# Performance work log

Hardware: AMD Instinct MI355X
Metric: run time of the kernel (lower is better)

## Reference

```python
import jax, jax.numpy as jnp
import numpy as np

B, S, HID = 2, 2048, 2048
H, HKV, D = 16, 4, 128

def _rope(x, cos, sin):
    # x: [B,h,S,D]; cos/sin: [1,1,S,D//2]
    d = x.shape[-1] // 2
    x1, x2 = x[..., :d], x[..., d:]
    y1 = x1 * cos + x2 * sin
    y2 = -x1 * sin + x2 * cos
    return jnp.concatenate([y1, y2], axis=-1)

def _rmsnorm(x):
    eps = jnp.finfo(x.dtype).eps
    return x * jax.lax.rsqrt(jnp.mean(jnp.square(x), axis=-1, keepdims=True) + eps)

def setup_inputs() -> dict:
    key = jax.random.key(0)
    ks = jax.random.split(key, 5)
    x = jax.random.normal(ks[0], (B, S, HID), dtype=jnp.float32)
    # realistic rotary tables
    half = D // 2
    inv_freq = 1.0 / (10000.0 ** (jnp.arange(half, dtype=jnp.float32) / half))
    t = jnp.arange(S, dtype=jnp.float32)
    freqs = t[:, None] * inv_freq[None, :]            # [S, D//2]
    cos = jnp.cos(freqs)[None, None]                  # [1,1,S,D//2]
    sin = jnp.sin(freqs)[None, None]
    s = 0.02
    Wq = jax.random.normal(ks[1], (H * D, HID), dtype=jnp.float32) * s
    Wk = jax.random.normal(ks[2], (HKV * D, HID), dtype=jnp.float32) * s
    Wv = jax.random.normal(ks[3], (HKV * D, HID), dtype=jnp.float32) * s
    Wo = jax.random.normal(ks[4], (HID, H * D), dtype=jnp.float32) * s
    return {"x": x, "cos": cos, "sin": sin, "Wq": Wq, "Wk": Wk, "Wv": Wv, "Wo": Wo}

def reference(x, cos, sin, Wq, Wk, Wv, Wo):
    b, s, _ = x.shape
    rep = H // HKV
    q = (x @ Wq.T).reshape(b, s, H, D).transpose(0, 2, 1, 3)      # [B,H,S,D]
    k = (x @ Wk.T).reshape(b, s, HKV, D).transpose(0, 2, 1, 3)    # [B,Hkv,S,D]
    v = (x @ Wv.T).reshape(b, s, HKV, D).transpose(0, 2, 1, 3)
    k = jnp.repeat(k, rep, axis=1)                                # GQA expand
    v = jnp.repeat(v, rep, axis=1)
    q = _rmsnorm(_rope(q, cos, sin))
    k = _rmsnorm(_rope(k, cos, sin))
    scores = jnp.einsum('bhqd,bhkd->bhqk', q, k) * (D ** -0.5)
    causal = jnp.tril(jnp.ones((s, s), dtype=bool))
    scores = jnp.where(causal, scores, -jnp.inf)
    attn = jax.nn.softmax(scores, axis=-1)
    out = jnp.einsum('bhqk,bhkd->bhqd', attn, v)                  # [B,H,S,D]
    out = out.transpose(0, 2, 1, 3).reshape(b, s, H * D)
    return out @ Wo.T
```

## Files before the change

### kernel.cpp

```cpp
#include <hip/hip_runtime.h>
#include <hip/hip_bf16.h>

#define B_  2
#define S_  2048
#define HID_ 2048
#define H_  16
#define HKV_ 4
#define D_  128

typedef __bf16 bf16_t;
typedef bf16_t bf16x8 __attribute__((ext_vector_type(8)));
typedef float f32x4 __attribute__((ext_vector_type(4)));

typedef __attribute__((address_space(3))) unsigned int lds_u32_t;
typedef const __attribute__((address_space(1))) unsigned int glob_u32_t;

__device__ __forceinline__ void gl2lds16(const bf16_t* g, bf16_t* l) {
    __builtin_amdgcn_global_load_lds((glob_u32_t*)g, (lds_u32_t*)l, 16, 0, 0);
}

__device__ __forceinline__ unsigned packbf2(float a, float b) {
    union { bf16_t h[2]; unsigned u; } p;
    p.h[0] = (bf16_t)a;
    p.h[1] = (bf16_t)b;
    return p.u;
}

__global__ void detect_dtype(const unsigned* __restrict__ x, int* __restrict__ flag) {
    int lane = threadIdx.x;
    int c = 0;
#pragma unroll
    for (int i = 0; i < 16; ++i) {
        unsigned w = x[lane * 16 + i];
        unsigned e = (w >> 7) & 0xFF;
        c += (e >= 117 && e <= 137) ? 1 : 0;
    }
#pragma unroll
    for (int m = 1; m < 64; m <<= 1) c += __shfl_xor(c, m, 64);
    if (lane == 0) *flag = (c >= 512) ? 1 : 0;
}

struct Cseg { const void* src; bf16_t* dst; int n8; };

__global__ __launch_bounds__(256) void convert_bf16(Cseg s0, Cseg s1, Cseg s2, Cseg s3,
                                                    const int* __restrict__ flagp) {
    Cseg s = (blockIdx.y == 0) ? s0 : (blockIdx.y == 1) ? s1 : (blockIdx.y == 2) ? s2 : s3;
    const int i = blockIdx.x * 256 + threadIdx.x;
    if (i >= s.n8) return;
    if (*flagp) {
        ((uint4*)s.dst)[i] = ((const uint4*)s.src)[i];
    } else {
        const float4* p = (const float4*)s.src + (size_t)i * 2;
        float4 u = p[0], v = p[1];
        bf16x8 r;
        r[0] = (bf16_t)u.x; r[1] = (bf16_t)u.y; r[2] = (bf16_t)u.z; r[3] = (bf16_t)u.w;
        r[4] = (bf16_t)v.x; r[5] = (bf16_t)v.y; r[6] = (bf16_t)v.z; r[7] = (bf16_t)v.w;
        *(bf16x8*)(s.dst + (size_t)i * 8) = r;
    }
}

__global__ __launch_bounds__(256) void gemm_lds(const bf16_t* __restrict__ A,
                                                const bf16_t* __restrict__ W,
                                                void* __restrict__ C,
                                                int M, int N, int K,
                                                const int* __restrict__ flagp, int osel) {
    __shared__ bf16_t As[128 * 32];
    __shared__ bf16_t Bs[128 * 32];

    const int tid = threadIdx.x;
    const int w = tid >> 6;
    const int lane = tid & 63;
    const int r = lane & 15;
    const int quad = lane >> 4;
    const int m0 = blockIdx.y * 128;
    const int n0 = blockIdx.x * 128;
    const bool of32 = osel && (*flagp == 0);

    const int mh = (w & 1) * 64;
    const int nh = (w >> 1) * 64;

    const int c0 = w * 2;
    const int srow = lane >> 2;
    const int scol = (lane & 3) * 8;
    const bf16_t* Ag0 = A + (size_t)(m0 + c0 * 16 + srow) * K + scol;
    const bf16_t* Ag1 = A + (size_t)(m0 + c0 * 16 + 16 + srow) * K + scol;
    const bf16_t* Wg0 = W + (size_t)(n0 + c0 * 16 + srow) * K + scol;
    const bf16_t* Wg1 = W + (size_t)(n0 + c0 * 16 + 16 + srow) * K + scol;
    bf16_t* Al0 = As + c0 * 512;
    bf16_t* Al1 = As + (c0 + 1) * 512;
    bf16_t* Bl0 = Bs + c0 * 512;
    bf16_t* Bl1 = Bs + (c0 + 1) * 512;

    f32x4 acc[4][4] = {};

    for (int k0 = 0; k0 < K; k0 += 32) {
        __syncthreads();
        gl2lds16(Ag0 + k0, Al0);
        gl2lds16(Ag1 + k0, Al1);
        gl2lds16(Wg0 + k0, Bl0);
        gl2lds16(Wg1 + k0, Bl1);
        __syncthreads();

        bf16x8 a[4], b[4];
#pragma unroll
        for (int mi = 0; mi < 4; ++mi)
            a[mi] = *(const bf16x8*)&As[(mh + mi * 16 + r) * 32 + quad * 8];
#pragma unroll
        for (int ni = 0; ni < 4; ++ni)
            b[ni] = *(const bf16x8*)&Bs[(nh + ni * 16 + r) * 32 + quad * 8];
#pragma unroll
        for (int mi = 0; mi < 4; ++mi)
#pragma unroll
            for (int ni = 0; ni < 4; ++ni)
                acc[mi][ni] = __builtin_amdgcn_mfma_f32_16x16x32_bf16(a[mi], b[ni], acc[mi][ni], 0, 0, 0);
    }

#pragma unroll
    for (int mi = 0; mi < 4; ++mi) {
#pragma unroll
        for (int ni = 0; ni < 4; ++ni) {
#pragma unroll
            for (int g = 0; g < 4; ++g) {
                const int row = m0 + mh + mi * 16 + quad * 4 + g;
                const int col = n0 + nh + ni * 16 + r;
                if (of32) ((float*)C)[(size_t)row * N + col] = acc[mi][ni][g];
                else ((__hip_bfloat16*)C)[(size_t)row * N + col] = __float2bfloat16(acc[mi][ni][g]);
            }
        }
    }
}

template <bool F32>
__device__ __forceinline__ bf16x8 load8(const void* base, size_t off) {
    bf16x8 r;
    if constexpr (F32) {
        const float4* p = (const float4*)((const float*)base + off);
        float4 u = p[0], v = p[1];
        r[0] = (bf16_t)u.x; r[1] = (bf16_t)u.y; r[2] = (bf16_t)u.z; r[3] = (bf16_t)u.w;
        r[4] = (bf16_t)v.x; r[5] = (bf16_t)v.y; r[6] = (bf16_t)v.z; r[7] = (bf16_t)v.w;
    } else {
        r = *(const bf16x8*)((const bf16_t*)base + off);
    }
    return r;
}

template <bool AF32, bool WF32, bool OF32>
__device__ __forceinline__ void gemm_body(const void* __restrict__ A, const void* __restrict__ W,
                                          void* __restrict__ C, int M, int N, int K) {
    const int wave = threadIdx.x >> 6;
    const int lane = threadIdx.x & 63;
    const int r = lane & 15;
    const int quad = lane >> 4;
    const int m0 = blockIdx.y * 64 + wave * 16;
    const int n0 = blockIdx.x * 64;

    f32x4 acc[4] = {};
    const size_t aoff = (size_t)(m0 + r) * K + quad * 8;
    const size_t woff = (size_t)(n0 + r) * K + quad * 8;

    for (int k0 = 0; k0 < K; k0 += 32) {
        bf16x8 a = load8<AF32>(A, aoff + k0);
#pragma unroll
        for (int ns = 0; ns < 4; ++ns) {
            bf16x8 b = load8<WF32>(W, woff + (size_t)(ns * 16) * K + k0);
            acc[ns] = __builtin_amdgcn_mfma_f32_16x16x32_bf16(a, b, acc[ns], 0, 0, 0);
        }
    }

#pragma unroll
    for (int ns = 0; ns < 4; ++ns) {
#pragma unroll
        for (int reg = 0; reg < 4; ++reg) {
            int m = m0 + quad * 4 + reg;
            int n = n0 + ns * 16 + r;
            if constexpr (OF32) ((float*)C)[(size_t)m * N + n] = acc[ns][reg];
            else ((__hip_bfloat16*)C)[(size_t)m * N + n] = __float2bfloat16(acc[ns][reg]);
        }
    }
}

__global__ __launch_bounds__(256) void gemm_bt(const void* __restrict__ A, const void* __restrict__ W,
                                               void* __restrict__ C, int M, int N, int K,
                                               const int* __restrict__ flagp, int mode) {
    const int bf = *flagp;
    if (bf) {
        gemm_body<false, false, false>(A, W, C, M, N, K);
    } else if (mode == 0) {
        gemm_body<true, true, false>(A, W, C, M, N, K);
    } else {
        gemm_body<false, true, true>(A, W, C, M, N, K);
    }
}

__global__ __launch_bounds__(256) void rope_rms(__hip_bfloat16* __restrict__ qk,
                                                const void* __restrict__ cosp,
                                                const void* __restrict__ sinp,
                                                int NH, int ld, const int* __restrict__ flagp) {
    const int bf = *flagp;
    const int wave = threadIdx.x >> 6;
    const int lane = threadIdx.x & 63;
    const int row = blockIdx.x * 4 + wave;
    const int h = row % NH;
    const int bs = row / NH;
    const int s = bs % S_;

    __hip_bfloat16* p = qk + (size_t)bs * ld + h * D_;
    float x1 = __bfloat162float(p[lane]);
    float x2 = __bfloat162float(p[lane + 64]);
    float c, sn, eps;
    if (bf) {
        c   = __bfloat162float(((const __hip_bfloat16*)cosp)[s * 64 + lane]);
        sn  = __bfloat162float(((const __hip_bfloat16*)sinp)[s * 64 + lane]);
        eps = 0.0078125f;
    } else {
        c   = ((const float*)cosp)[s * 64 + lane];
        sn  = ((const float*)sinp)[s * 64 + lane];
        eps = 1.1920929e-07f;
    }
    float y1 = x1 * c + x2 * sn;
    float y2 = x2 * c - x1 * sn;
    float ss = y1 * y1 + y2 * y2;
#pragma unroll
    for (int m = 1; m < 64; m <<= 1) ss += __shfl_xor(ss, m, 64);
    float rinv = rsqrtf(ss * (1.0f / 128.0f) + eps);
    p[lane]      = __float2bfloat16(y1 * rinv);
    p[lane + 64] = __float2bfloat16(y2 * rinv);
}

#define KT_ 32
#define LDK 136

__global__ __launch_bounds__(256, 2) void attn_flash3(const __hip_bfloat16* __restrict__ Q,
                                                      const __hip_bfloat16* __restrict__ K,
                                                      const __hip_bfloat16* __restrict__ V,
                                                      __hip_bfloat16* __restrict__ O,
                                                      int ldq, int ldkv, int ldo) {
    __shared__ unsigned short Ks[KT_][LDK];
    __shared__ unsigned int Vt[D_ * 16];
    __shared__ unsigned int Pb[4][2][16][16];

    const int tid = threadIdx.x;
    const int w = tid >> 6;
    const int lane = tid & 63;
    const int r = lane & 15;
    const int quad = lane >> 4;

    const int gy = blockIdx.y;
    const int kvh = gy % HKV_;
    const int b = gy / HKV_;
    const int qt = b ? blockIdx.x : (gridDim.x - 1 - blockIdx.x);
    const int q0 = qt * 32;
    const int h = kvh * 4 + w;

    bf16x8 qf[2][4];
#pragma unroll
    for (int t = 0; t < 2; ++t) {
        const bf16_t* qp = (const bf16_t*)Q + (size_t)(b * S_ + q0 + t * 16 + r) * ldq + h * D_ + quad * 8;
#pragma unroll
        for (int c = 0; c < 4; ++c) qf[t][c] = *(const bf16x8*)(qp + c * 32);
    }

    f32x4 oacc[2][8] = {};
    f32x4 lacc[2] = {};
    float m_i[2][4];
#pragma unroll
    for (int t = 0; t < 2; ++t)
#pragma unroll
        for (int g = 0; g < 4; ++g) m_i[t][g] = -3e38f;

    const bf16_t* Kg = (const bf16_t*)K + (size_t)b * S_ * ldkv + kvh * D_;
    const bf16_t* Vg = (const bf16_t*)V + (size_t)b * S_ * ldkv + kvh * D_;

    bf16x8 ones;
#pragma unroll
    for (int j = 0; j < 8; ++j) ones[j] = (bf16_t)1.0f;

    const float SC2 = 0.08838834764831845f * 1.4426950408889634f;

    const int skey = tid >> 4;
    const int sdc = tid & 15;
    union U4 { uint4 u; unsigned short s[8]; };
    U4 rk0, rk1, rv0, rv1;
    {
        const size_t o0 = (size_t)skey * ldkv + sdc * 8;
        const size_t o1 = o0 + (size_t)16 * ldkv;
        rk0.u = *(const uint4*)(Kg + o0);
        rk1.u = *(const uint4*)(Kg + o1);
        rv0.u = *(const uint4*)(Vg + o0);
        rv1.u = *(const uint4*)(Vg + o1);
    }

    for (int kt = 0; kt <= qt; ++kt) {
        const int k0 = kt * KT_;
        __syncthreads();
        *(uint4*)&Ks[skey][sdc * 8] = rk0.u;
        *(uint4*)&Ks[skey + 16][sdc * 8] = rk1.u;
#pragma unroll
        for (int j = 0; j < 8; ++j) {
            const int d = sdc * 8 + j;
            const int f = ((j >> 1) & 3) ^ (sdc & 3);
            const int grp = (skey >> 2) ^ f;
            Vt[d * 16 + grp * 4 + (skey & 3)] = (unsigned)rv0.s[j] | ((unsigned)rv1.s[j] << 16);
        }
        __syncthreads();
        if (kt < qt) {
            const size_t o0 = (size_t)(k0 + KT_ + skey) * ldkv + sdc * 8;
            const size_t o1 = o0 + (size_t)16 * ldkv;
            rk0.u = *(const uint4*)(Kg + o0);
            rk1.u = *(const uint4*)(Kg + o1);
            rv0.u = *(const uint4*)(Vg + o0);
            rv1.u = *(const uint4*)(Vg + o1);
        }

        f32x4 s0[2] = {}, s1[2] = {};
#pragma unroll
        for (int c = 0; c < 4; ++c) {
            bf16x8 kb0 = *(const bf16x8*)&Ks[r][c * 32 + quad * 8];
            bf16x8 kb1 = *(const bf16x8*)&Ks[16 + r][c * 32 + quad * 8];
#pragma unroll
            for (int t = 0; t < 2; ++t) {
                s0[t] = __builtin_amdgcn_mfma_f32_16x16x32_bf16(qf[t][c], kb0, s0[t], 0, 0, 0);
                s1[t] = __builtin_amdgcn_mfma_f32_16x16x32_bf16(qf[t][c], kb1, s1[t], 0, 0, 0);
            }
        }

        const bool bnd = (kt == qt);
#pragma unroll
        for (int t = 0; t < 2; ++t) {
            float mt[4];
#pragma unroll
            for (int g = 0; g < 4; ++g) {
                s0[t][g] *= SC2;
                s1[t][g] *= SC2;
                if (bnd) {
                    const int qrow = q0 + t * 16 + quad * 4 + g;
                    if (k0 + r > qrow)      s0[t][g] = -1e38f;
                    if (k0 + 16 + r > qrow) s1[t][g] = -1e38f;
                }
                mt[g] = fmaxf(s0[t][g], s1[t][g]);
            }
#pragma unroll
            for (int msk = 1; msk < 16; msk <<= 1) {
#pragma unroll
                for (int g = 0; g < 4; ++g) mt[g] = fmaxf(mt[g], __shfl_xor(mt[g], msk, 64));
            }
            bool upd = false;
#pragma unroll
            for (int g = 0; g < 4; ++g) upd |= (mt[g] > m_i[t][g]);
            if (__ballot(upd)) {
#pragma unroll
                for (int g = 0; g < 4; ++g) {
                    const float mn = fmaxf(m_i[t][g], mt[g]);
                    const float al = exp2f(m_i[t][g] - mn);
                    m_i[t][g] = mn;
                    lacc[t][g] *= al;
#pragma unroll
                    for (int ns = 0; ns < 8; ++ns) oacc[t][ns][g] *= al;
                }
            }
#pragma unroll
            for (int g = 0; g < 4; ++g) {
                const float p0 = exp2f(s0[t][g] - m_i[t][g]);
                const float p1 = exp2f(s1[t][g] - m_i[t][g]);
                const int row = quad * 4 + g;
                Pb[w][t][row][(((r >> 2) ^ quad) & 3) * 4 + (r & 3)] = packbf2(p0, p1);
            }
        }

        const int pgrp = ((quad ^ (r >> 2)) & 3) * 4;
        bf16x8 pf0 = *(const bf16x8*)&Pb[w][0][r][pgrp];
        bf16x8 pf1 = *(const bf16x8*)&Pb[w][1][r][pgrp];

        lacc[0] = __builtin_amdgcn_mfma_f32_16x16x32_bf16(pf0, ones, lacc[0], 0, 0, 0);
        lacc[1] = __builtin_amdgcn_mfma_f32_16x16x32_bf16(pf1, ones, lacc[1], 0, 0, 0);

#pragma unroll
        for (int ns = 0; ns < 8; ++ns) {
            const int d = ns * 16 + r;
            const int f = ((r >> 1) & 3) ^ ((2 * ns + (r >> 3)) & 3);
            bf16x8 vf = *(const bf16x8*)&Vt[d * 16 + ((quad ^ f) & 3) * 4];
            oacc[0][ns] = __builtin_amdgcn_mfma_f32_16x16x32_bf16(pf0, vf, oacc[0][ns], 0, 0, 0);
            oacc[1][ns] = __builtin_amdgcn_mfma_f32_16x16x32_bf16(pf1, vf, oacc[1][ns], 0, 0, 0);
        }
    }

#pragma unroll
    for (int t = 0; t < 2; ++t) {
#pragma unroll
        for (int g = 0; g < 4; ++g) {
            const float inv = 1.0f / lacc[t][g];
            const int qrow = q0 + t * 16 + quad * 4 + g;
            __hip_bfloat16* op = O + (size_t)(b * S_ + qrow) * ldo + h * D_;
#pragma unroll
            for (int ns = 0; ns < 8; ++ns)
                op[ns * 16 + r] = __float2bfloat16(oacc[t][ns][g] * inv);
        }
    }
}

extern "C" void kernel_launch(void* const* d_in, const int* in_sizes, int n_in,
                              void* d_out, int out_size, void* d_ws, size_t ws_size,
                              hipStream_t stream) {
    const void* x    = d_in[0];
    const void* cosp = d_in[1];
    const void* sinp = d_in[2];
    const void* Wq   = d_in[3];
    const void* Wk   = d_in[4];
    const void* Wv   = d_in[5];
    const void* Wo   = d_in[6];

    const int M = B_ * S_;
    const size_t MB = 1ull << 20;

    if (ws_size >= 28 * MB + 64) {
        char* ws = (char*)d_ws;
        bf16_t* xb = (bf16_t*)ws;
        bf16_t* wb = (bf16_t*)(ws + 16 * MB);
        bf16_t* wo = (bf16_t*)(ws + 16 * MB);
        bf16_t* ao = (bf16_t*)ws;
        int* flag  = (int*)(ws + 28 * MB);
        bf16_t* qkv = (bf16_t*)d_out;

        detect_dtype<<<1, 64, 0, stream>>>((const unsigned*)x, flag);

        Cseg sx{x,  xb,                          (B_ * S_ * HID_) / 8};
        Cseg sq{Wq, wb,                          (H_ * D_ * HID_) / 8};
        Cseg sk{Wk, wb + (size_t)2048 * HID_,    (HKV_ * D_ * HID_) / 8};
        Cseg sv{Wv, wb + (size_t)2560 * HID_,    (HKV_ * D_ * HID_) / 8};
        convert_bf16<<<dim3(4096, 4), 256, 0, stream>>>(sx, sq, sk, sv, flag);

        gemm_lds<<<dim3(3072 / 128, M / 128), 256, 0, stream>>>(xb, wb, qkv, M, 3072, HID_, flag, 0);

        Cseg so{Wo, wo, (HID_ * H_ * D_) / 8};
        convert_bf16<<<dim3(2048, 1), 256, 0, stream>>>(so, so, so, so, flag);

        rope_rms<<<(B_ * S_ * H_) / 4, 256, 0, stream>>>((__hip_bfloat16*)qkv, cosp, sinp, H_, 3072, flag);
        rope_rms<<<(B_ * S_ * HKV_) / 4, 256, 0, stream>>>((__hip_bfloat16*)(qkv + 2048), cosp, sinp, HKV_, 3072, flag);

        attn_flash3<<<dim3(S_ / 32, B_ * HKV_), 256, 0, stream>>>(
            (const __hip_bfloat16*)qkv, (const __hip_bfloat16*)(qkv + 2048),
            (const __hip_bfloat16*)(qkv + 2560), (__hip_bfloat16*)ao, 3072, 3072, 2048);

        gemm_lds<<<dim3(HID_ / 128, M / 128), 256, 0, stream>>>(ao, wo, d_out, M, HID_, H_ * D_, flag, 1);
    } else {
        __hip_bfloat16* qb = (__hip_bfloat16*)d_ws;
        int* flag = (int*)((char*)d_ws + (size_t)M * (H_ * D_) * sizeof(__hip_bfloat16));
        __hip_bfloat16* kb = (__hip_bfloat16*)d_out;
        __hip_bfloat16* vb = kb + (size_t)M * (HKV_ * D_);

        detect_dtype<<<1, 64, 0, stream>>>((const unsigned*)x, flag);

        gemm_bt<<<dim3((H_ * D_) / 64, M / 64), 256, 0, stream>>>(x, Wq, qb, M, H_ * D_, HID_, flag, 0);
        gemm_bt<<<dim3((HKV_ * D_) / 64, M / 64), 256, 0, stream>>>(x, Wk, kb, M, HKV_ * D_, HID_, flag, 0);
        gemm_bt<<<dim3((HKV_ * D_) / 64, M / 64), 256, 0, stream>>>(x, Wv, vb, M, HKV_ * D_, HID_, flag, 0);

        rope_rms<<<(B_ * S_ * H_) / 4, 256, 0, stream>>>(qb, cosp, sinp, H_, H_ * D_, flag);
        rope_rms<<<(B_ * S_ * HKV_) / 4, 256, 0, stream>>>(kb, cosp, sinp, HKV_, HKV_ * D_, flag);

        attn_flash3<<<dim3(S_ / 32, B_ * HKV_), 256, 0, stream>>>(qb, kb, vb, qb, H_ * D_, HKV_ * D_, H_ * D_);

        gemm_bt<<<dim3(HID_ / 64, M / 64), 256, 0, stream>>>(qb, Wo, d_out, M, HID_, H_ * D_, flag, 1);
    }
}
```

Before: 417.9 us.

## Add split-KV flash attention with pre-packed V and causal load balancing

Adds a v_pack kernel that rearranges V into a pre-transposed, pair-packed layout so the attention kernel can load MFMA B-operands straight from global memory without an LDS transpose. A new attn_flash4 kernel uses 512 threads: each of the four KV-group heads gets two waves that split the key range in half, and the halves are merged through LDS with a log-sum-exp combine. Each block processes a pair of query tiles (qt and 63-qt) to balance causal work across blocks. K and V are read from global memory rather than staged in LDS, which relies on cache hits, and the extra pack kernel and merge step add overhead.

```diff
diff --git a/kernel.cpp b/kernel.cpp
--- a/kernel.cpp
+++ b/kernel.cpp
@@ -227,6 +227,202 @@
     p[lane + 64] = __float2bfloat16(y2 * rinv);
 }
 
+__global__ __launch_bounds__(256) void v_pack(const __hip_bfloat16* __restrict__ V,
+                                              unsigned* __restrict__ Vp, int ldv) {
+    const int idx = blockIdx.x * 256 + threadIdx.x;
+    const int kp = idx & 15;
+    const int t  = (idx >> 4) & 63;
+    const int d  = (idx >> 10) & 127;
+    const int gy = idx >> 17;
+    const int kvh = gy & 3;
+    const int b = gy >> 2;
+    const unsigned short* p = (const unsigned short*)V
+        + (size_t)(b * S_ + 32 * t + kp) * ldv + kvh * D_ + d;
+    unsigned lo = p[0];
+    unsigned hi = p[(size_t)16 * ldv];
+    Vp[idx] = lo | (hi << 16);
+}
+
+__global__ __launch_bounds__(512, 2) void attn_flash4(const __hip_bfloat16* __restrict__ Q,
+                                                      const __hip_bfloat16* __restrict__ K,
+                                                      const unsigned* __restrict__ Vp,
+                                                      __hip_bfloat16* __restrict__ O,
+                                                      int ldq, int ldkv, int ldo) {
+    __shared__ unsigned Pb[8][2][16][16];
+    __shared__ float Of[4][32][128];
+    __shared__ float Ml[4][2][2][16];
+
+    const int tid = threadIdx.x;
+    const int w = tid >> 6;
+    const int lane = tid & 63;
+    const int r = lane & 15;
+    const int quad = lane >> 4;
+
+    const int id = blockIdx.x;
+    const int gy = id & 7;
+    const int px = id >> 3;
+    const int kvh = gy & 3;
+    const int b = gy >> 2;
+    const int hh = w & 3;
+    const int half = w >> 2;
+    const int h = kvh * 4 + hh;
+
+    const bf16_t* Kg = (const bf16_t*)K + (size_t)b * S_ * ldkv + kvh * D_;
+    const unsigned* Vg = Vp + (size_t)gy * (D_ * 64 * 16);
+
+    bf16x8 ones;
+#pragma unroll
+    for (int j = 0; j < 8; ++j) ones[j] = (bf16_t)1.0f;
+
+    const float SC2 = 0.08838834764831845f * 1.4426950408889634f;
+
+    for (int rep = 0; rep < 2; ++rep) {
+        const int qt = rep ? (63 - px) : px;
+        const int q0 = qt * 32;
+        const int nkt = qt + 1;
+        const int ktb = half ? (nkt >> 1) : 0;
+        const int kte = half ? nkt : (nkt >> 1);
+
+        bf16x8 qf[2][4];
+#pragma unroll
+        for (int t = 0; t < 2; ++t) {
+            const bf16_t* qp = (const bf16_t*)Q + (size_t)(b * S_ + q0 + t * 16 + r) * ldq + h * D_ + quad * 8;
+#pragma unroll
+            for (int c = 0; c < 4; ++c) qf[t][c] = *(const bf16x8*)(qp + c * 32);
+        }
+
+        f32x4 oacc[2][8] = {};
+        f32x4 lacc[2] = {};
+        float m_i[2][4];
+#pragma unroll
+        for (int t = 0; t < 2; ++t)
+#pragma unroll
+            for (int g = 0; g < 4; ++g) m_i[t][g] = -3e38f;
+
+        for (int kt = ktb; kt < kte; ++kt) {
+            const int k0 = kt * 32;
+            const bf16_t* kp0 = Kg + (size_t)(k0 + r) * ldkv + quad * 8;
+
+            f32x4 s0[2] = {}, s1[2] = {};
+            __builtin_amdgcn_s_setprio(1);
+#pragma unroll
+            for (int c = 0; c < 4; ++c) {
+                bf16x8 kb0 = *(const bf16x8*)(kp0 + c * 32);
+                bf16x8 kb1 = *(const bf16x8*)(kp0 + (size_t)16 * ldkv + c * 32);
+#pragma unroll
+                for (int t = 0; t < 2; ++t) {
+                    s0[t] = __builtin_amdgcn_mfma_f32_16x16x32_bf16(qf[t][c], kb0, s0[t], 0, 0, 0);
+                    s1[t] = __builtin_amdgcn_mfma_f32_16x16x32_bf16(qf[t][c], kb1, s1[t], 0, 0, 0);
+                }
+            }
+            __builtin_amdgcn_s_setprio(0);
+
+            const bool bnd = (kt == qt);
+#pragma unroll
+            for (int t = 0; t < 2; ++t) {
+                float mt[4];
+#pragma unroll
+                for (int g = 0; g < 4; ++g) {
+                    s0[t][g] *= SC2;
+                    s1[t][g] *= SC2;
+                    if (bnd) {
+                        const int qrow = q0 + t * 16 + quad * 4 + g;
+                        if (k0 + r > qrow)      s0[t][g] = -1e38f;
+                        if (k0 + 16 + r > qrow) s1[t][g] = -1e38f;
+                    }
+                    mt[g] = fmaxf(s0[t][g], s1[t][g]);
+                }
+#pragma unroll
+                for (int msk = 1; msk < 16; msk <<= 1) {
+#pragma unroll
+                    for (int g = 0; g < 4; ++g) mt[g] = fmaxf(mt[g], __shfl_xor(mt[g], msk, 64));
+                }
+                bool upd = false;
+#pragma unroll
+                for (int g = 0; g < 4; ++g) upd |= (mt[g] > m_i[t][g]);
+                if (__ballot(upd)) {
+#pragma unroll
+                    for (int g = 0; g < 4; ++g) {
+                        const float mn = fmaxf(m_i[t][g], mt[g]);
+                        const float al = exp2f(m_i[t][g] - mn);
+                        m_i[t][g] = mn;
+                        lacc[t][g] *= al;
+#pragma unroll
+                        for (int ns = 0; ns < 8; ++ns) oacc[t][ns][g] *= al;
+                    }
+                }
+#pragma unroll
+                for (int g = 0; g < 4; ++g) {
+                    const float p0 = exp2f(s0[t][g] - m_i[t][g]);
+                    const float p1 = exp2f(s1[t][g] - m_i[t][g]);
+                    const int row = quad * 4 + g;
+                    Pb[w][t][row][(((r >> 2) ^ quad) & 3) * 4 + (r & 3)] = packbf2(p0, p1);
+                }
+            }
+
+            const int pgrp = ((quad ^ (r >> 2)) & 3) * 4;
+            bf16x8 pf0 = *(const bf16x8*)&Pb[w][0][r][pgrp];
+            bf16x8 pf1 = *(const bf16x8*)&Pb[w][1][r][pgrp];
+
+            lacc[0] = __builtin_amdgcn_mfma_f32_16x16x32_bf16(pf0, ones, lacc[0], 0, 0, 0);
+            lacc[1] = __builtin_amdgcn_mfma_f32_16x16x32_bf16(pf1, ones, lacc[1], 0, 0, 0);
+
+            const unsigned* vp = Vg + (size_t)r * (64 * 16) + kt * 16 + quad * 4;
+            __builtin_amdgcn_s_setprio(1);
+#pragma unroll
+            for (int ns = 0; ns < 8; ++ns) {
+                bf16x8 vf = *(const bf16x8*)(vp + (size_t)ns * 16 * 64 * 16);
+                oacc[0][ns] = __builtin_amdgcn_mfma_f32_16x16x32_bf16(pf0, vf, oacc[0][ns], 0, 0, 0);
+                oacc[1][ns] = __builtin_amdgcn_mfma_f32_16x16x32_bf16(pf1, vf, oacc[1][ns], 0, 0, 0);
+            }
+            __builtin_amdgcn_s_setprio(0);
+        }
+
+        if (half) {
+#pragma unroll
+            for (int t = 0; t < 2; ++t) {
+                if (r == 0) {
+#pragma unroll
+                    for (int g = 0; g < 4; ++g) {
+                        Ml[hh][t][0][quad * 4 + g] = m_i[t][g];
+                        Ml[hh][t][1][quad * 4 + g] = lacc[t][g];
+                    }
+                }
+#pragma unroll
+                for (int ns = 0; ns < 8; ++ns)
+#pragma unroll
+                    for (int g = 0; g < 4; ++g)
+                        Of[hh][t * 16 + quad * 4 + g][ns * 16 + r] = oacc[t][ns][g];
+            }
+        }
+        __syncthreads();
+        if (!half) {
+#pragma unroll
+            for (int t = 0; t < 2; ++t) {
+#pragma unroll
+                for (int g = 0; g < 4; ++g) {
+                    const int r16 = quad * 4 + g;
+                    const float mB = Ml[hh][t][0][r16];
+                    const float lB = Ml[hh][t][1][r16];
+                    const float mA = m_i[t][g];
+                    const float mx = fmaxf(mA, mB);
+                    const float aA = exp2f(mA - mx);
+                    const float aB = exp2f(mB - mx);
+                    const float inv = 1.0f / (lacc[t][g] * aA + lB * aB);
+                    const int qrow = q0 + t * 16 + r16;
+                    __hip_bfloat16* op = O + (size_t)(b * S_ + qrow) * ldo + h * D_;
+#pragma unroll
+                    for (int ns = 0; ns < 8; ++ns) {
+                        const float v = (oacc[t][ns][g] * aA + Of[hh][t * 16 + r16][ns * 16 + r] * aB) * inv;
+                        op[ns * 16 + r] = __float2bfloat16(v);
+                    }
+                }
+            }
+        }
+        __syncthreads();
+    }
+}
+
 #define KT_ 32
 #define LDK 136
 
@@ -417,6 +613,7 @@
         bf16_t* xb = (bf16_t*)ws;
         bf16_t* wb = (bf16_t*)(ws + 16 * MB);
         bf16_t* wo = (bf16_t*)(ws + 16 * MB);
+        unsigned* vp4 = (unsigned*)(ws + 24 * MB);
         bf16_t* ao = (bf16_t*)ws;
         int* flag  = (int*)(ws + 28 * MB);
         bf16_t* qkv = (bf16_t*)d_out;
@@ -434,12 +631,15 @@
         Cseg so{Wo, wo, (HID_ * H_ * D_) / 8};
         convert_bf16<<<dim3(2048, 1), 256, 0, stream>>>(so, so, so, so, flag);
 
+        v_pack<<<(B_ * HKV_ * D_ * 64 * 16) / 256, 256, 0, stream>>>(
+            (const __hip_bfloat16*)(qkv + 2560), vp4, 3072);
+
         rope_rms<<<(B_ * S_ * H_) / 4, 256, 0, stream>>>((__hip_bfloat16*)qkv, cosp, sinp, H_, 3072, flag);
         rope_rms<<<(B_ * S_ * HKV_) / 4, 256, 0, stream>>>((__hip_bfloat16*)(qkv + 2048), cosp, sinp, HKV_, 3072, flag);
 
-        attn_flash3<<<dim3(S_ / 32, B_ * HKV_), 256, 0, stream>>>(
+        attn_flash4<<<dim3(256), 512, 0, stream>>>(
             (const __hip_bfloat16*)qkv, (const __hip_bfloat16*)(qkv + 2048),
-            (const __hip_bfloat16*)(qkv + 2560), (__hip_bfloat16*)ao, 3072, 3072, 2048);
+            vp4, (__hip_bfloat16*)ao, 3072, 3072, 2048);
 
         gemm_lds<<<dim3(HID_ / 128, M / 128), 256, 0, stream>>>(ao, wo, d_out, M, HID_, H_ * D_, flag, 1);
     } else {
```

Result: no change. 416.9 us (-0.3%).

## Pre-pack K/V into MFMA-friendly layouts and use register-direct flash attention kernel

Applied to the files above, without the earlier changes.

Adds k_pack and v_pack kernels that reorder K tiles and pair-interleave V rows so each wave can load MFMA operands straight from global memory into registers, with no LDS staging. A new attn_flash6 kernel runs 8 waves per block with load-balanced causal tile pairing and double-buffered K/V register loads. It skips online max tracking by using a fixed exponent offset, which is valid because q and k are RMS-normalised and the score is bounded. The row sum is computed with an MFMA against a ones vector. The cost is two extra packing passes and more register pressure.

```diff
diff --git a/kernel.cpp b/kernel.cpp
--- a/kernel.cpp
+++ b/kernel.cpp
@@ -227,6 +227,194 @@
     p[lane + 64] = __float2bfloat16(y2 * rinv);
 }
 
+__global__ __launch_bounds__(256) void k_pack(const __hip_bfloat16* __restrict__ Kin,
+                                              bf16_t* __restrict__ Kp) {
+    const int idx = blockIdx.x * 256 + threadIdx.x;
+    const int d0 = (idx & 15) * 8;
+    const int row = (idx >> 4) & 31;
+    const int kt = (idx >> 9) & 63;
+    const int gy = idx >> 15;
+    const int kvh = gy & 3;
+    const int bb = gy >> 2;
+    const bf16_t* src = (const bf16_t*)Kin + (size_t)(bb * S_ + kt * 32 + row) * 3072 + kvh * D_ + d0;
+    *(uint4*)(Kp + (size_t)idx * 8) = *(const uint4*)src;
+}
+
+__global__ __launch_bounds__(256) void v_pack(const __hip_bfloat16* __restrict__ V,
+                                              unsigned* __restrict__ Vp, int ldv) {
+    const int idx = blockIdx.x * 256 + threadIdx.x;
+    const int kp = idx & 15;
+    const int d  = (idx >> 4) & 127;
+    const int kt = (idx >> 11) & 63;
+    const int gy = idx >> 17;
+    const int kvh = gy & 3;
+    const int b = gy >> 2;
+    const unsigned short* p = (const unsigned short*)V
+        + (size_t)(b * S_ + 32 * kt + kp) * ldv + kvh * D_ + d;
+    unsigned lo = p[0];
+    unsigned hi = p[(size_t)16 * ldv];
+    Vp[idx] = lo | (hi << 16);
+}
+
+#define M0F 16.5f
+
+__global__ __launch_bounds__(512, 2) void attn_flash6(const __hip_bfloat16* __restrict__ Q,
+                                                      const bf16_t* __restrict__ Kp,
+                                                      const unsigned* __restrict__ Vp,
+                                                      __hip_bfloat16* __restrict__ O) {
+    __shared__ unsigned PbS[8][2][16][16];
+    __shared__ bf16_t  Os[8][32][136];
+
+    const int tid = threadIdx.x;
+    const int w = tid >> 6;
+    const int lane = tid & 63;
+    const int r = lane & 15;
+    const int quad = lane >> 4;
+
+    const int id = blockIdx.x;
+    const int gy = id & 7;
+    const int u = id >> 3;
+    const int hh = u & 3;
+    const int i = u >> 2;
+    const int kvh = gy & 3;
+    const int b = gy >> 2;
+    const int h = kvh * 4 + hh;
+
+    const int s4 = w & 3;
+    int tlo = (s4 == 0) ? i : (s4 == 1) ? (31 - i) : (s4 == 2) ? (16 + i) : (15 - i);
+    const int qt = (w < 4) ? tlo : (63 - tlo);
+    const int q0 = qt * 32;
+
+    const bf16_t* Kg = Kp + (size_t)gy * (64 * 32 * 128);
+    const unsigned* Vg = Vp + (size_t)gy * (64 * 128 * 16);
+
+    bf16x8 qf[2][4];
+#pragma unroll
+    for (int t = 0; t < 2; ++t) {
+        const bf16_t* qp = (const bf16_t*)Q + (size_t)(b * S_ + q0 + t * 16 + r) * 3072 + h * D_ + quad * 8;
+#pragma unroll
+        for (int c = 0; c < 4; ++c) qf[t][c] = *(const bf16x8*)(qp + c * 32);
+    }
+
+    f32x4 oacc[2][8] = {};
+    f32x4 lacc[2] = {};
+
+    bf16x8 ones;
+#pragma unroll
+    for (int j = 0; j < 8; ++j) ones[j] = (bf16_t)1.0f;
+
+    const float SC2 = 0.08838834764831845f * 1.4426950408889634f;
+
+    unsigned* pbw = &PbS[w][0][0][0];
+    const int pwi = (((r >> 2) ^ quad) & 3) * 4 + (r & 3);
+    const int pgrp = ((quad ^ (r >> 2)) & 3) * 4;
+
+    bf16x8 ka[8], va[8], kb[8], vb[8];
+
+#define LOADKV(KB, VB, KT) do {                                               \
+        const bf16_t* kp_ = Kg + (size_t)(KT) * 4096 + r * 128 + quad * 8;    \
+        const unsigned* vp_ = Vg + (size_t)(KT) * 2048 + r * 16 + quad * 4;   \
+        KB[0] = *(const bf16x8*)(kp_);                                        \
+        KB[1] = *(const bf16x8*)(kp_ + 2048);                                 \
+        KB[2] = *(const bf16x8*)(kp_ + 32);                                   \
+        KB[3] = *(const bf16x8*)(kp_ + 2048 + 32);                            \
+        KB[4] = *(const bf16x8*)(kp_ + 64);                                   \
+        KB[5] = *(const bf16x8*)(kp_ + 2048 + 64);                            \
+        KB[6] = *(const bf16x8*)(kp_ + 96);                                   \
+        KB[7] = *(const bf16x8*)(kp_ + 2048 + 96);                            \
+        VB[0] = *(const bf16x8*)(vp_);                                        \
+        VB[1] = *(const bf16x8*)(vp_ + 256);                                  \
+        VB[2] = *(const bf16x8*)(vp_ + 512);                                  \
+        VB[3] = *(const bf16x8*)(vp_ + 768);                                  \
+        VB[4] = *(const bf16x8*)(vp_ + 1024);                                 \
+        VB[5] = *(const bf16x8*)(vp_ + 1280);                                 \
+        VB[6] = *(const bf16x8*)(vp_ + 1536);                                 \
+        VB[7] = *(const bf16x8*)(vp_ + 1792);                                 \
+    } while (0)
+
+#define COMPUTE(KB, VB, KT) do {                                              \
+        f32x4 s0_[2] = {}, s1_[2] = {};                                       \
+        __builtin_amdgcn_s_setprio(1);                                        \
+        _Pragma("unroll")                                                     \
+        for (int c = 0; c < 4; ++c) {                                         \
+            _Pragma("unroll")                                                 \
+            for (int t = 0; t < 2; ++t) {                                     \
+                s0_[t] = __builtin_amdgcn_mfma_f32_16x16x32_bf16(qf[t][c], KB[c * 2], s0_[t], 0, 0, 0);     \
+                s1_[t] = __builtin_amdgcn_mfma_f32_16x16x32_bf16(qf[t][c], KB[c * 2 + 1], s1_[t], 0, 0, 0); \
+            }                                                                 \
+        }                                                                     \
+        __builtin_amdgcn_s_setprio(0);                                        \
+        if ((KT) == qt) {                                                     \
+            _Pragma("unroll")                                                 \
+            for (int t = 0; t < 2; ++t)                                       \
+                _Pragma("unroll")                                             \
+                for (int g = 0; g < 4; ++g) {                                 \
+                    const int qrow_ = q0 + t * 16 + quad * 4 + g;             \
+                    if ((KT) * 32 + r > qrow_)      s0_[t][g] = -1e38f;       \
+                    if ((KT) * 32 + 16 + r > qrow_) s1_[t][g] = -1e38f;       \
+                }                                                             \
+        }                                                                     \
+        _Pragma("unroll")                                                     \
+        for (int t = 0; t < 2; ++t)                                           \
+            _Pragma("unroll")                                                 \
+            for (int g = 0; g < 4; ++g) {                                     \
+                const float p0_ = exp2f(fmaf(s0_[t][g], SC2, -M0F));          \
+                const float p1_ = exp2f(fmaf(s1_[t][g], SC2, -M0F));          \
+                pbw[t * 256 + (quad * 4 + g) * 16 + pwi] = packbf2(p0_, p1_); \
+            }                                                                 \
+        bf16x8 pf0_ = *(const bf16x8*)&pbw[r * 16 + pgrp];                    \
+        bf16x8 pf1_ = *(const bf16x8*)&pbw[256 + r * 16 + pgrp];              \
+        lacc[0] = __builtin_amdgcn_mfma_f32_16x16x32_bf16(pf0_, ones, lacc[0], 0, 0, 0); \
+        lacc[1] = __builtin_amdgcn_mfma_f32_16x16x32_bf16(pf1_, ones, lacc[1], 0, 0, 0); \
+        __builtin_amdgcn_s_setprio(1);                                        \
+        _Pragma("unroll")                                                     \
+        for (int ns = 0; ns < 8; ++ns) {                                      \
+            oacc[0][ns] = __builtin_amdgcn_mfma_f32_16x16x32_bf16(pf0_, VB[ns], oacc[0][ns], 0, 0, 0); \
+            oacc[1][ns] = __builtin_amdgcn_mfma_f32_16x16x32_bf16(pf1_, VB[ns], oacc[1][ns], 0, 0, 0); \
+        }                                                                     \
+        __builtin_amdgcn_s_setprio(0);                                        \
+    } while (0)
+
+    LOADKV(ka, va, 0);
+    int kt = 0;
+    for (;;) {
+        if (kt < qt) LOADKV(kb, vb, kt + 1);
+        COMPUTE(ka, va, kt);
+        if (++kt > qt) break;
+        if (kt < qt) LOADKV(ka, va, kt + 1);
+        COMPUTE(kb, vb, kt);
+        if (++kt > qt) break;
+    }
+
+    float inv[2][4];
+#pragma unroll
+    for (int t = 0; t < 2; ++t)
+#pragma unroll
+        for (int g = 0; g < 4; ++g) inv[t][g] = 1.0f / lacc[t][g];
+
+#pragma unroll
+    for (int t = 0; t < 2; ++t)
+#pragma unroll
+        for (int g = 0; g < 4; ++g) {
+            const int row = t * 16 + quad * 4 + g;
+#pragma unroll
+            for (int ns = 0; ns < 8; ++ns)
+                Os[w][row][ns * 16 + r] = (bf16_t)(oacc[t][ns][g] * inv[t][g]);
+        }
+
+    bf16_t* ob = (bf16_t*)O + (size_t)(b * S_ + q0) * 2048 + h * D_;
+#pragma unroll
+    for (int c = 0; c < 8; ++c) {
+        const int idx2 = c * 64 + lane;
+        const int row = idx2 >> 4;
+        const int seg = idx2 & 15;
+        bf16x8 v8 = *(const bf16x8*)&Os[w][row][seg * 8];
+        *(bf16x8*)(ob + (size_t)row * 2048 + seg * 8) = v8;
+    }
+#undef LOADKV
+#undef COMPUTE
+}
+
 #define KT_ 32
 #define LDK 136
 
@@ -417,9 +605,11 @@
         bf16_t* xb = (bf16_t*)ws;
         bf16_t* wb = (bf16_t*)(ws + 16 * MB);
         bf16_t* wo = (bf16_t*)(ws + 16 * MB);
+        unsigned* vp4 = (unsigned*)(ws + 24 * MB);
         bf16_t* ao = (bf16_t*)ws;
         int* flag  = (int*)(ws + 28 * MB);
         bf16_t* qkv = (bf16_t*)d_out;
+        bf16_t* kp8 = (bf16_t*)((char*)d_out + 24 * MB);
 
         detect_dtype<<<1, 64, 0, stream>>>((const unsigned*)x, flag);
 
@@ -434,12 +624,16 @@
         Cseg so{Wo, wo, (HID_ * H_ * D_) / 8};
         convert_bf16<<<dim3(2048, 1), 256, 0, stream>>>(so, so, so, so, flag);
 
+        v_pack<<<(B_ * HKV_ * D_ * 64 * 16) / 256, 256, 0, stream>>>(
+            (const __hip_bfloat16*)(qkv + 2560), vp4, 3072);
+
         rope_rms<<<(B_ * S_ * H_) / 4, 256, 0, stream>>>((__hip_bfloat16*)qkv, cosp, sinp, H_, 3072, flag);
         rope_rms<<<(B_ * S_ * HKV_) / 4, 256, 0, stream>>>((__hip_bfloat16*)(qkv + 2048), cosp, sinp, HKV_, 3072, flag);
 
-        attn_flash3<<<dim3(S_ / 32, B_ * HKV_), 256, 0, stream>>>(
-            (const __hip_bfloat16*)qkv, (const __hip_bfloat16*)(qkv + 2048),
-            (const __hip_bfloat16*)(qkv + 2560), (__hip_bfloat16*)ao, 3072, 3072, 2048);
+        k_pack<<<dim3(1024), 256, 0, stream>>>((const __hip_bfloat16*)(qkv + 2048), kp8);
+
+        attn_flash6<<<dim3(256), 512, 0, stream>>>(
+            (const __hip_bfloat16*)qkv, kp8, vp4, (__hip_bfloat16*)ao);
 
         gemm_lds<<<dim3(HID_ / 128, M / 128), 256, 0, stream>>>(ao, wo, d_out, M, HID_, H_ * D_, flag, 1);
     } else {
```

After: 540.0 us. +29.2%, slower.
